# Performance work log

Measured on AMD Instinct MI355X. Metric: run time of the kernel, lower is better.

The kernel has to match this reference:

```python
import jax, jax.numpy as jnp
import numpy as np

EPS = 1e-12


def _complex_log(x):
    # log of a real tensor as a complex number: log|x| + i*pi*[x<0]
    real = jnp.log(jnp.maximum(jnp.abs(x), EPS))
    imag = jnp.where(x < 0, jnp.pi, 0.0).astype(jnp.float32)
    return jax.lax.complex(real.astype(jnp.float32), imag)


def _logcumsumexp_complex(x, axis):
    # numerically-stable complex logcumsumexp via associative scan
    def logaddexp_c(a, b):
        m = jnp.maximum(a.real, b.real)  # real-valued max for stability
        return jnp.log(jnp.exp(a - m) + jnp.exp(b - m)) + m
    return jax.lax.associative_scan(logaddexp_c, x, axis=axis)


def setup_inputs() -> dict:
    key = jax.random.key(0)
    ks = jax.random.split(key, 7)
    b, d, l, n = 2, 1024, 1024, 16
    u = jax.random.normal(ks[0], (b, d, l), dtype=jnp.float32)
    delta = jax.random.normal(ks[1], (b, d, l), dtype=jnp.float32)
    # A negative (like Mamba's A = -exp(A_log)) so the scan stays stable
    A = -(0.5 + jax.random.uniform(ks[2], (d, n), dtype=jnp.float32))
    B = jax.random.normal(ks[3], (b, n, l), dtype=jnp.float32)
    C = jax.random.normal(ks[4], (b, n, l), dtype=jnp.float32)
    D = jax.random.normal(ks[5], (d,), dtype=jnp.float32)
    z = jax.random.normal(ks[6], (b, d, l), dtype=jnp.float32)
    return {"u": u, "delta": delta, "A": A, "B": B, "C": C, "D": D, "z": z}


def reference(u, delta, A, B, C, D, z):
    # delta_softplus=True path of SelectiveScanTorch.forward
    dt = jax.nn.softplus(delta)                                   # (b,d,l)
    dA = jnp.einsum('bdl,dn->bldn', dt, A)                        # (b,l,d,n)
    dB_u = jnp.einsum('bdl,bdl,bnl->bldn', dt, u, B)              # (b,l,d,n)

    dB_u_log = _complex_log(dB_u)                                 # complex64
    # dA_star[l] = sum_{k=1}^{l} dA[k]  (exclusive of step 0, front-padded)
    dA_star = jnp.pad(jnp.cumsum(dA[:, 1:], axis=1),
                      ((0, 0), (1, 0), (0, 0), (0, 0)))
    x_log = _logcumsumexp_complex(dB_u_log - dA_star, axis=1) + dA_star

    x_real = jnp.exp(x_log.real) * jnp.cos(x_log.imag)            # (b,l,d,n)
    y = jnp.einsum('bldn,bnl->bdl', x_real.astype(C.dtype), C)    # (b,d,l)
    out = y + u * D[None, :, None]
    return (out * jax.nn.silu(z)).astype(u.dtype)
```

## Files before the change

### kernel.cpp

```cpp
#include <hip/hip_runtime.h>
#include <math.h>

namespace {

constexpr int kD = 1024;
constexpr int kL = 1024;
constexpr int kN = 16;
constexpr int kE = 4;
constexpr int kJ = 8;
constexpr int kT = 512;
constexpr int kC = 256;
constexpr int kCP = kC + 1;

__device__ __forceinline__ float rfl(float x) {
    return __uint_as_float(__builtin_amdgcn_readfirstlane(__float_as_uint(x)));
}

__global__ __launch_bounds__(kT)
void selscan(const float* __restrict__ u,
             const float* __restrict__ delta,
             const float* __restrict__ A,
             const float* __restrict__ Bm,
             const float* __restrict__ Cm,
             const float* __restrict__ Dv,
             const float* __restrict__ z,
             float* __restrict__ out)
{
    __shared__ float2 sax[kN][kCP];
    __shared__ float2 sw[8][kN];
    __shared__ float2 syr[kC][3];

    const int bd   = blockIdx.x;
    const int b    = bd >> 10;
    const int d    = bd & (kD - 1);
    const int t    = threadIdx.x;
    const int lane = t & 63;
    const int wave = t >> 6;
    const int nh   = wave >> 2;
    const int n0   = nh << 3;
    const int chunk = ((wave & 3) << 6) | lane;
    const int l0   = chunk << 2;
    const size_t base = (size_t)bd * kL;

    const float LOG2E = 1.4426950408889634f;
    const float LN2   = 0.6931471805599453f;

    float dt2[kE], dtu[kE];
    {
        float4 dv = *(const float4*)(delta + base + l0);
        float4 uv = *(const float4*)(u + base + l0);
        float dd[4] = {dv.x, dv.y, dv.z, dv.w};
        float uu[4] = {uv.x, uv.y, uv.z, uv.w};
        #pragma unroll
        for (int s = 0; s < kE; ++s) {
            float x = dd[s];
            float e = __builtin_amdgcn_exp2f(-fabsf(x) * LOG2E);
            float sp = fmaxf(x, 0.f) + __builtin_amdgcn_logf(1.f + e) * LN2;
            dt2[s] = sp * LOG2E;
            dtu[s] = sp * uu[s];
        }
    }

    float aj[kJ];
    {
        const float* Ap = A + d * kN + n0;
        #pragma unroll
        for (int j = 0; j < kJ; ++j) aj[j] = rfl(Ap[j]);
    }

    float Q[kJ][kE];
    float y[kE] = {0.f, 0.f, 0.f, 0.f};
    const int rowbase = (b << 4) + n0;
    #pragma unroll
    for (int j = 0; j < kJ; ++j) {
        const float* Bp = Bm + (size_t)(rowbase + j) * kL + l0;
        const float* Cp = Cm + (size_t)(rowbase + j) * kL + l0;
        float4 b4 = *(const float4*)Bp;
        float4 c4 = *(const float4*)Cp;
        float Bv[4] = {b4.x, b4.y, b4.z, b4.w};
        float Cv[4] = {c4.x, c4.y, c4.z, c4.w};
        float x = 0.f, p = 1.f;
        #pragma unroll
        for (int s = 0; s < kE; ++s) {
            float e = __builtin_amdgcn_exp2f(dt2[s] * aj[j]);
            x = fmaf(e, x, dtu[s] * Bv[s]);
            p *= e;
            Q[j][s] = p * Cv[s];
            y[s] = fmaf(x, Cv[s], y[s]);
        }
        sax[n0 + j][chunk] = make_float2(p, x);
    }
    __syncthreads();

    {
        const int sn = lane & 15;
        const int q  = lane >> 4;
        const int cb = (wave << 5) + (q << 3);

        float p = 1.f, c = 0.f;
        #pragma unroll
        for (int i = 0; i < 8; ++i) {
            float2 ax = sax[sn][cb + i];
            c = fmaf(ax.x, c, ax.y);
            p *= ax.x;
        }
        float Aq = p, Xq = c;
        {
            float ain = __shfl_up(Aq, 16, 64);
            float xin = __shfl_up(Xq, 16, 64);
            bool act = (lane >= 16);
            Xq = fmaf(Aq, act ? xin : 0.f, Xq);
            Aq *= act ? ain : 1.f;
            ain = __shfl_up(Aq, 32, 64);
            xin = __shfl_up(Xq, 32, 64);
            act = (lane >= 32);
            Xq = fmaf(Aq, act ? xin : 0.f, Xq);
            Aq *= act ? ain : 1.f;
        }
        if (q == 3) sw[wave][sn] = make_float2(Aq, Xq);
        float eA = __shfl_up(Aq, 16, 64);
        float eX = __shfl_up(Xq, 16, 64);
        if (lane < 16) { eA = 1.f; eX = 0.f; }
        __syncthreads();

        float wx = 0.f;
        #pragma unroll
        for (int w = 0; w < 7; ++w) {
            if (w < wave) {
                float2 s2 = sw[w][sn];
                wx = fmaf(s2.x, wx, s2.y);
            }
        }
        float cc = fmaf(eA, wx, eX);
        #pragma unroll
        for (int i = 0; i < 8; ++i) {
            float2 ax = sax[sn][cb + i];
            sax[sn][cb + i].x = cc;
            cc = fmaf(ax.x, cc, ax.y);
        }
    }
    __syncthreads();

    #pragma unroll
    for (int j = 0; j < kJ; ++j) {
        float carry = sax[n0 + j][chunk].x;
        #pragma unroll
        for (int s = 0; s < kE; ++s)
            y[s] = fmaf(carry, Q[j][s], y[s]);
    }

    if (nh == 1) {
        syr[chunk][0] = make_float2(y[0], y[1]);
        syr[chunk][1] = make_float2(y[2], y[3]);
    }
    __syncthreads();

    if (nh == 0) {
        float2 ya = syr[chunk][0];
        float2 yb = syr[chunk][1];
        float y0 = y[0] + ya.x;
        float y1 = y[1] + ya.y;
        float y2 = y[2] + yb.x;
        float y3 = y[3] + yb.y;

        const float D_d = rfl(Dv[d]);
        float4 uv = *(const float4*)(u + base + l0);
        float4 zv = *(const float4*)(z + base + l0);
        float s0 = __builtin_amdgcn_rcpf(1.f + __builtin_amdgcn_exp2f(-zv.x * LOG2E));
        float s1 = __builtin_amdgcn_rcpf(1.f + __builtin_amdgcn_exp2f(-zv.y * LOG2E));
        float s2 = __builtin_amdgcn_rcpf(1.f + __builtin_amdgcn_exp2f(-zv.z * LOG2E));
        float s3 = __builtin_amdgcn_rcpf(1.f + __builtin_amdgcn_exp2f(-zv.w * LOG2E));
        float4 o;
        o.x = (y0 + uv.x * D_d) * zv.x * s0;
        o.y = (y1 + uv.y * D_d) * zv.y * s1;
        o.z = (y2 + uv.z * D_d) * zv.z * s2;
        o.w = (y3 + uv.w * D_d) * zv.w * s3;
        *(float4*)(out + base + l0) = o;
    }
}

}

extern "C" void kernel_launch(void* const* d_in, const int* in_sizes, int n_in,
                              void* d_out, int out_size, void* d_ws, size_t ws_size,
                              hipStream_t stream) {
    const float* u     = (const float*)d_in[0];
    const float* delta = (const float*)d_in[1];
    const float* A     = (const float*)d_in[2];
    const float* Bm    = (const float*)d_in[3];
    const float* Cm    = (const float*)d_in[4];
    const float* Dv    = (const float*)d_in[5];
    const float* z     = (const float*)d_in[6];
    float* out = (float*)d_out;

    dim3 grid(2 * kD);
    dim3 block(kT);
    hipLaunchKernelGGL(selscan, grid, block, 0, stream,
                       u, delta, A, Bm, Cm, Dv, z, out);
}
```

Before: 22.01 us.

## Split state dimension scan into two rounds to cut register pressure

Processes the 8 per-thread state columns in two rounds of 4. Each round runs its own local recurrence, shared-memory cross-chunk scan and carry application. This halves the live Q array and may lower VGPR use enough to raise occupancy. In exchange it doubles the number of block-wide barriers and scan phases, and the cross-lane scan gains an extra shuffle step.

After: 25.83 us. 1.17x slower.

```diff
diff --git a/kernel.cpp b/kernel.cpp
--- a/kernel.cpp
+++ b/kernel.cpp
@@ -7,7 +7,8 @@
 constexpr int kL = 1024;
 constexpr int kN = 16;
 constexpr int kE = 4;
-constexpr int kJ = 8;
+constexpr int kJ = 4;
+constexpr int kR = 2;
 constexpr int kT = 512;
 constexpr int kC = 256;
 constexpr int kCP = kC + 1;
@@ -26,8 +27,8 @@
              const float* __restrict__ z,
              float* __restrict__ out)
 {
-    __shared__ float2 sax[kN][kCP];
-    __shared__ float2 sw[8][kN];
+    __shared__ float2 sax[kR][8][kCP];
+    __shared__ float2 sw[8][8];
     __shared__ float2 syr[kC][3];
 
     const int bd   = blockIdx.x;
@@ -61,92 +62,93 @@
         }
     }
 
-    float aj[kJ];
+    float aj[2 * kJ];
     {
         const float* Ap = A + d * kN + n0;
         #pragma unroll
-        for (int j = 0; j < kJ; ++j) aj[j] = rfl(Ap[j]);
-    }
-
-    float Q[kJ][kE];
+        for (int j = 0; j < 2 * kJ; ++j) aj[j] = rfl(Ap[j]);
+    }
+
     float y[kE] = {0.f, 0.f, 0.f, 0.f};
     const int rowbase = (b << 4) + n0;
+
     #pragma unroll
-    for (int j = 0; j < kJ; ++j) {
-        const float* Bp = Bm + (size_t)(rowbase + j) * kL + l0;
-        const float* Cp = Cm + (size_t)(rowbase + j) * kL + l0;
-        float4 b4 = *(const float4*)Bp;
-        float4 c4 = *(const float4*)Cp;
-        float Bv[4] = {b4.x, b4.y, b4.z, b4.w};
-        float Cv[4] = {c4.x, c4.y, c4.z, c4.w};
-        float x = 0.f, p = 1.f;
-        #pragma unroll
-        for (int s = 0; s < kE; ++s) {
-            float e = __builtin_amdgcn_exp2f(dt2[s] * aj[j]);
-            x = fmaf(e, x, dtu[s] * Bv[s]);
-            p *= e;
-            Q[j][s] = p * Cv[s];
-            y[s] = fmaf(x, Cv[s], y[s]);
-        }
-        sax[n0 + j][chunk] = make_float2(p, x);
-    }
-    __syncthreads();
-
-    {
-        const int sn = lane & 15;
-        const int q  = lane >> 4;
-        const int cb = (wave << 5) + (q << 3);
-
-        float p = 1.f, c = 0.f;
-        #pragma unroll
-        for (int i = 0; i < 8; ++i) {
-            float2 ax = sax[sn][cb + i];
-            c = fmaf(ax.x, c, ax.y);
-            p *= ax.x;
-        }
-        float Aq = p, Xq = c;
+    for (int r = 0; r < kR; ++r) {
+        float Q[kJ][kE];
+        #pragma unroll
+        for (int jj = 0; jj < kJ; ++jj) {
+            const int j = (r << 2) + jj;
+            const float* Bp = Bm + (size_t)(rowbase + j) * kL + l0;
+            const float* Cp = Cm + (size_t)(rowbase + j) * kL + l0;
+            float4 b4 = *(const float4*)Bp;
+            float4 c4 = *(const float4*)Cp;
+            float Bv[4] = {b4.x, b4.y, b4.z, b4.w};
+            float Cv[4] = {c4.x, c4.y, c4.z, c4.w};
+            float x = 0.f, p = 1.f;
+            #pragma unroll
+            for (int s = 0; s < kE; ++s) {
+                float e = __builtin_amdgcn_exp2f(dt2[s] * aj[j]);
+                x = fmaf(e, x, dtu[s] * Bv[s]);
+                p *= e;
+                Q[jj][s] = p * Cv[s];
+                y[s] = fmaf(x, Cv[s], y[s]);
+            }
+            sax[r][(nh << 2) + jj][chunk] = make_float2(p, x);
+        }
+        __syncthreads();
+
         {
-            float ain = __shfl_up(Aq, 16, 64);
-            float xin = __shfl_up(Xq, 16, 64);
-            bool act = (lane >= 16);
-            Xq = fmaf(Aq, act ? xin : 0.f, Xq);
-            Aq *= act ? ain : 1.f;
-            ain = __shfl_up(Aq, 32, 64);
-            xin = __shfl_up(Xq, 32, 64);
-            act = (lane >= 32);
-            Xq = fmaf(Aq, act ? xin : 0.f, Xq);
-            Aq *= act ? ain : 1.f;
-        }
-        if (q == 3) sw[wave][sn] = make_float2(Aq, Xq);
-        float eA = __shfl_up(Aq, 16, 64);
-        float eX = __shfl_up(Xq, 16, 64);
-        if (lane < 16) { eA = 1.f; eX = 0.f; }
+            const int sn = lane & 7;
+            const int q  = lane >> 3;
+            const int cb = (wave << 5) + (q << 2);
+
+            float p = 1.f, c = 0.f;
+            #pragma unroll
+            for (int i = 0; i < 4; ++i) {
+                float2 ax = sax[r][sn][cb + i];
+                c = fmaf(ax.x, c, ax.y);
+                p *= ax.x;
+            }
+            float Aq = p, Xq = c;
+            #pragma unroll
+            for (int dlt = 8; dlt <= 32; dlt <<= 1) {
+                float ain = __shfl_up(Aq, dlt, 64);
+                float xin = __shfl_up(Xq, dlt, 64);
+                bool act = (lane >= dlt);
+                Xq = fmaf(Aq, act ? xin : 0.f, Xq);
+                Aq *= act ? ain : 1.f;
+            }
+            if (q == 7) sw[wave][sn] = make_float2(Aq, Xq);
+            float eA = __shfl_up(Aq, 8, 64);
+            float eX = __shfl_up(Xq, 8, 64);
+            if (lane < 8) { eA = 1.f; eX = 0.f; }
+            __syncthreads();
+
+            float wx = 0.f;
+            #pragma unroll
+            for (int w = 0; w < 7; ++w) {
+                if (w < wave) {
+                    float2 s2 = sw[w][sn];
+                    wx = fmaf(s2.x, wx, s2.y);
+                }
+            }
+            float cc = fmaf(eA, wx, eX);
+            #pragma unroll
+            for (int i = 0; i < 4; ++i) {
+                float2 ax = sax[r][sn][cb + i];
+                sax[r][sn][cb + i].x = cc;
+                cc = fmaf(ax.x, cc, ax.y);
+            }
+        }
         __syncthreads();
 
-        float wx = 0.f;
-        #pragma unroll
-        for (int w = 0; w < 7; ++w) {
-            if (w < wave) {
-                float2 s2 = sw[w][sn];
-                wx = fmaf(s2.x, wx, s2.y);
-            }
-        }
-        float cc = fmaf(eA, wx, eX);
-        #pragma unroll
-        for (int i = 0; i < 8; ++i) {
-            float2 ax = sax[sn][cb + i];
-            sax[sn][cb + i].x = cc;
-            cc = fmaf(ax.x, cc, ax.y);
-        }
-    }
-    __syncthreads();
-
-    #pragma unroll
-    for (int j = 0; j < kJ; ++j) {
-        float carry = sax[n0 + j][chunk].x;
-        #pragma unroll
-        for (int s = 0; s < kE; ++s)
-            y[s] = fmaf(carry, Q[j][s], y[s]);
+        #pragma unroll
+        for (int jj = 0; jj < kJ; ++jj) {
+            float carry = sax[r][(nh << 2) + jj][chunk].x;
+            #pragma unroll
+            for (int s = 0; s < kE; ++s)
+                y[s] = fmaf(carry, Q[jj][s], y[s]);
+        }
     }
 
     if (nh == 1) {
```

## Split state dimension across four wave groups with 1024-thread blocks

Applied to the files above, without the earlier changes.

Doubles the block to 1024 threads so each thread handles 4 state channels instead of 8, and widens the cross-wave scan to 16 waves of 4 chunks each. The final y reduction now sums partials from four groups through shared memory. B/C loads are software-prefetched one row ahead inside the state loop. This roughly halves per-thread serial work and register pressure, at the cost of a longer cross-wave carry chain, more shared-memory traffic for the reduction, and fewer resident blocks per CU.

Measured after the change: 32.32 us. 46.9% more time.

```diff
diff --git a/kernel.cpp b/kernel.cpp
--- a/kernel.cpp
+++ b/kernel.cpp
@@ -7,8 +7,8 @@
 constexpr int kL = 1024;
 constexpr int kN = 16;
 constexpr int kE = 4;
-constexpr int kJ = 8;
-constexpr int kT = 512;
+constexpr int kJ = 4;
+constexpr int kT = 1024;
 constexpr int kC = 256;
 constexpr int kCP = kC + 1;
 
@@ -27,8 +27,8 @@
              float* __restrict__ out)
 {
     __shared__ float2 sax[kN][kCP];
-    __shared__ float2 sw[8][kN];
-    __shared__ float2 syr[kC][3];
+    __shared__ float2 sw[16][kN];
+    __shared__ float2 syr[6][kC];
 
     const int bd   = blockIdx.x;
     const int b    = bd >> 10;
@@ -36,8 +36,8 @@
     const int t    = threadIdx.x;
     const int lane = t & 63;
     const int wave = t >> 6;
-    const int nh   = wave >> 2;
-    const int n0   = nh << 3;
+    const int ng   = wave >> 2;
+    const int n0   = ng << 2;
     const int chunk = ((wave & 3) << 6) | lane;
     const int l0   = chunk << 2;
     const size_t base = (size_t)bd * kL;
@@ -71,35 +71,37 @@
     float Q[kJ][kE];
     float y[kE] = {0.f, 0.f, 0.f, 0.f};
     const int rowbase = (b << 4) + n0;
+    float4 b4 = *(const float4*)(Bm + (size_t)rowbase * kL + l0);
+    float4 c4 = *(const float4*)(Cm + (size_t)rowbase * kL + l0);
     #pragma unroll
-    for (int j = 0; j < kJ; ++j) {
-        const float* Bp = Bm + (size_t)(rowbase + j) * kL + l0;
-        const float* Cp = Cm + (size_t)(rowbase + j) * kL + l0;
-        float4 b4 = *(const float4*)Bp;
-        float4 c4 = *(const float4*)Cp;
+    for (int jj = 0; jj < kJ; ++jj) {
         float Bv[4] = {b4.x, b4.y, b4.z, b4.w};
         float Cv[4] = {c4.x, c4.y, c4.z, c4.w};
+        if (jj < kJ - 1) {
+            b4 = *(const float4*)(Bm + (size_t)(rowbase + jj + 1) * kL + l0);
+            c4 = *(const float4*)(Cm + (size_t)(rowbase + jj + 1) * kL + l0);
+        }
         float x = 0.f, p = 1.f;
         #pragma unroll
         for (int s = 0; s < kE; ++s) {
-            float e = __builtin_amdgcn_exp2f(dt2[s] * aj[j]);
+            float e = __builtin_amdgcn_exp2f(dt2[s] * aj[jj]);
             x = fmaf(e, x, dtu[s] * Bv[s]);
             p *= e;
-            Q[j][s] = p * Cv[s];
+            Q[jj][s] = p * Cv[s];
             y[s] = fmaf(x, Cv[s], y[s]);
         }
-        sax[n0 + j][chunk] = make_float2(p, x);
+        sax[n0 + jj][chunk] = make_float2(p, x);
     }
     __syncthreads();
 
     {
         const int sn = lane & 15;
         const int q  = lane >> 4;
-        const int cb = (wave << 5) + (q << 3);
+        const int cb = (wave << 4) + (q << 2);
 
         float p = 1.f, c = 0.f;
         #pragma unroll
-        for (int i = 0; i < 8; ++i) {
+        for (int i = 0; i < 4; ++i) {
             float2 ax = sax[sn][cb + i];
             c = fmaf(ax.x, c, ax.y);
             p *= ax.x;
@@ -125,7 +127,7 @@
 
         float wx = 0.f;
         #pragma unroll
-        for (int w = 0; w < 7; ++w) {
+        for (int w = 0; w < 15; ++w) {
             if (w < wave) {
                 float2 s2 = sw[w][sn];
                 wx = fmaf(s2.x, wx, s2.y);
@@ -133,7 +135,7 @@
         }
         float cc = fmaf(eA, wx, eX);
         #pragma unroll
-        for (int i = 0; i < 8; ++i) {
+        for (int i = 0; i < 4; ++i) {
             float2 ax = sax[sn][cb + i];
             sax[sn][cb + i].x = cc;
             cc = fmaf(ax.x, cc, ax.y);
@@ -142,26 +144,27 @@
     __syncthreads();
 
     #pragma unroll
-    for (int j = 0; j < kJ; ++j) {
-        float carry = sax[n0 + j][chunk].x;
+    for (int jj = 0; jj < kJ; ++jj) {
+        float carry = sax[n0 + jj][chunk].x;
         #pragma unroll
         for (int s = 0; s < kE; ++s)
-            y[s] = fmaf(carry, Q[j][s], y[s]);
-    }
-
-    if (nh == 1) {
-        syr[chunk][0] = make_float2(y[0], y[1]);
-        syr[chunk][1] = make_float2(y[2], y[3]);
+            y[s] = fmaf(carry, Q[jj][s], y[s]);
+    }
+
+    if (ng != 0) {
+        syr[2 * ng - 2][chunk] = make_float2(y[0], y[1]);
+        syr[2 * ng - 1][chunk] = make_float2(y[2], y[3]);
     }
     __syncthreads();
 
-    if (nh == 0) {
-        float2 ya = syr[chunk][0];
-        float2 yb = syr[chunk][1];
-        float y0 = y[0] + ya.x;
-        float y1 = y[1] + ya.y;
-        float y2 = y[2] + yb.x;
-        float y3 = y[3] + yb.y;
+    if (ng == 0) {
+        float2 a0 = syr[0][chunk], a1 = syr[1][chunk];
+        float2 b0 = syr[2][chunk], b1 = syr[3][chunk];
+        float2 c0 = syr[4][chunk], c1 = syr[5][chunk];
+        float y0 = y[0] + a0.x + b0.x + c0.x;
+        float y1 = y[1] + a0.y + b0.y + c0.y;
+        float y2 = y[2] + a1.x + b1.x + c1.x;
+        float y3 = y[3] + a1.y + b1.y + c1.y;
 
         const float D_d = rfl(Dv[d]);
         float4 uv = *(const float4*)(u + base + l0);
```

## Split epilogue across both wave halves and prefetch B/C rows and z early

Applied to the files above, without the earlier changes.

The final reduction and output epilogue is now shared by both n-halves: each half exchanges two partial y values through shared memory and writes a float2 of output, instead of one half doing all four. z is loaded at kernel start and u is kept in registers rather than reloaded. B and C rows are software-prefetched one iteration ahead inside the state loop. The aim is to balance the tail work, hide global-load latency, and remove redundant loads, at the cost of narrower float2 stores and slightly higher register pressure.

New measurement: 31.27 us. 1.42x slower.

```diff
diff --git a/kernel.cpp b/kernel.cpp
--- a/kernel.cpp
+++ b/kernel.cpp
@@ -28,7 +28,7 @@
 {
     __shared__ float2 sax[kN][kCP];
     __shared__ float2 sw[8][kN];
-    __shared__ float2 syr[kC][3];
+    __shared__ float2 syr[2][kC];
 
     const int bd   = blockIdx.x;
     const int b    = bd >> 10;
@@ -45,7 +45,10 @@
     const float LOG2E = 1.4426950408889634f;
     const float LN2   = 0.6931471805599453f;
 
+    float2 zv2 = *(const float2*)(z + base + l0 + 2 * nh);
+
     float dt2[kE], dtu[kE];
+    float ue0, ue1;
     {
         float4 dv = *(const float4*)(delta + base + l0);
         float4 uv = *(const float4*)(u + base + l0);
@@ -59,6 +62,8 @@
             dt2[s] = sp * LOG2E;
             dtu[s] = sp * uu[s];
         }
+        ue0 = nh ? uu[2] : uu[0];
+        ue1 = nh ? uu[3] : uu[1];
     }
 
     float aj[kJ];
@@ -71,14 +76,16 @@
     float Q[kJ][kE];
     float y[kE] = {0.f, 0.f, 0.f, 0.f};
     const int rowbase = (b << 4) + n0;
+    float4 b4 = *(const float4*)(Bm + (size_t)rowbase * kL + l0);
+    float4 c4 = *(const float4*)(Cm + (size_t)rowbase * kL + l0);
     #pragma unroll
     for (int j = 0; j < kJ; ++j) {
-        const float* Bp = Bm + (size_t)(rowbase + j) * kL + l0;
-        const float* Cp = Cm + (size_t)(rowbase + j) * kL + l0;
-        float4 b4 = *(const float4*)Bp;
-        float4 c4 = *(const float4*)Cp;
         float Bv[4] = {b4.x, b4.y, b4.z, b4.w};
         float Cv[4] = {c4.x, c4.y, c4.z, c4.w};
+        if (j < kJ - 1) {
+            b4 = *(const float4*)(Bm + (size_t)(rowbase + j + 1) * kL + l0);
+            c4 = *(const float4*)(Cm + (size_t)(rowbase + j + 1) * kL + l0);
+        }
         float x = 0.f, p = 1.f;
         #pragma unroll
         for (int s = 0; s < kE; ++s) {
@@ -149,34 +156,21 @@
             y[s] = fmaf(carry, Q[j][s], y[s]);
     }
 
-    if (nh == 1) {
-        syr[chunk][0] = make_float2(y[0], y[1]);
-        syr[chunk][1] = make_float2(y[2], y[3]);
-    }
+    if (nh == 0) syr[0][chunk] = make_float2(y[2], y[3]);
+    else         syr[1][chunk] = make_float2(y[0], y[1]);
     __syncthreads();
 
-    if (nh == 0) {
-        float2 ya = syr[chunk][0];
-        float2 yb = syr[chunk][1];
-        float y0 = y[0] + ya.x;
-        float y1 = y[1] + ya.y;
-        float y2 = y[2] + yb.x;
-        float y3 = y[3] + yb.y;
+    float2 oth = syr[nh ^ 1][chunk];
+    float ya = (nh ? y[2] : y[0]) + oth.x;
+    float yb = (nh ? y[3] : y[1]) + oth.y;
 
-        const float D_d = rfl(Dv[d]);
-        float4 uv = *(const float4*)(u + base + l0);
-        float4 zv = *(const float4*)(z + base + l0);
-        float s0 = __builtin_amdgcn_rcpf(1.f + __builtin_amdgcn_exp2f(-zv.x * LOG2E));
-        float s1 = __builtin_amdgcn_rcpf(1.f + __builtin_amdgcn_exp2f(-zv.y * LOG2E));
-        float s2 = __builtin_amdgcn_rcpf(1.f + __builtin_amdgcn_exp2f(-zv.z * LOG2E));
-        float s3 = __builtin_amdgcn_rcpf(1.f + __builtin_amdgcn_exp2f(-zv.w * LOG2E));
-        float4 o;
-        o.x = (y0 + uv.x * D_d) * zv.x * s0;
-        o.y = (y1 + uv.y * D_d) * zv.y * s1;
-        o.z = (y2 + uv.z * D_d) * zv.z * s2;
-        o.w = (y3 + uv.w * D_d) * zv.w * s3;
-        *(float4*)(out + base + l0) = o;
-    }
+    const float D_d = rfl(Dv[d]);
+    float s0 = __builtin_amdgcn_rcpf(1.f + __builtin_amdgcn_exp2f(-zv2.x * LOG2E));
+    float s1 = __builtin_amdgcn_rcpf(1.f + __builtin_amdgcn_exp2f(-zv2.y * LOG2E));
+    float2 o;
+    o.x = (ya + ue0 * D_d) * zv2.x * s0;
+    o.y = (yb + ue1 * D_d) * zv2.y * s1;
+    *(float2*)(out + base + l0 + 2 * nh) = o;
 }
 
 }
```
